# Optimization experiments

Measured on AMD Instinct MI355X. Metric: run time of the kernel, lower is better.

The kernel has to match this reference:

```python
import jax, jax.numpy as jnp
import numpy as np

B, S, D, H = 4, 1024, 2048, 16
HD = D // H
SCALE = float(np.sqrt(HD))


def setup_inputs() -> dict:
    key = jax.random.key(0)
    ks = jax.random.split(key, 11)
    std = 1.0 / np.sqrt(D)
    inp = {
        'q': jax.random.normal(ks[0], (B, S, D), jnp.float32),
        'k': jax.random.normal(ks[1], (B, S, D), jnp.float32),
        'v': jax.random.normal(ks[2], (B, S, D), jnp.float32),
        'wq_w': jax.random.uniform(ks[3], (D, D), jnp.float32, -std, std),
        'wq_b': jax.random.uniform(ks[4], (D,), jnp.float32, -std, std),
        'wk_w': jax.random.uniform(ks[5], (D, D), jnp.float32, -std, std),
        'wk_b': jax.random.uniform(ks[6], (D,), jnp.float32, -std, std),
        'wv_w': jax.random.uniform(ks[7], (D, D), jnp.float32, -std, std),
        'wv_b': jax.random.uniform(ks[8], (D,), jnp.float32, -std, std),
        'wo_w': jax.random.uniform(ks[9], (D, D), jnp.float32, -std, std),
        'wo_b': jax.random.uniform(ks[10], (D,), jnp.float32, -std, std),
    }
    return inp


def reference(q, k, v, wq_w, wq_b, wk_w, wk_b, wv_w, wv_b, wo_w, wo_b):
    # Linear projections (torch Linear: x @ W.T + b), split into heads: [B,H,S,HD]
    Q = (q @ wq_w.T + wq_b).reshape(B, S, H, HD).transpose(0, 2, 1, 3)
    K = (k @ wk_w.T + wk_b).reshape(B, S, H, HD).transpose(0, 2, 1, 3)
    V = (v @ wv_w.T + wv_b).reshape(B, S, H, HD).transpose(0, 2, 1, 3)
    # scaled dot-product attention; mask=None, dropout identity (eval)
    scores = jnp.einsum('bhqd,bhkd->bhqk', Q, K) / SCALE  # [B,H,S,S]
    attn = jax.nn.softmax(scores, axis=-1)
    context = jnp.einsum('bhqk,bhkd->bhqd', attn, V)      # [B,H,S,HD]
    context = context.transpose(0, 2, 1, 3).reshape(B, S, D)
    output = context @ wo_w.T + wo_b
    return output, attn
```

## Files before the change

kernel.cpp:

```cpp
#include <hip/hip_runtime.h>
#include <hip/hip_bf16.h>


typedef __attribute__((ext_vector_type(4)))  float f32x4;
typedef __attribute__((ext_vector_type(16))) float f32x16;
typedef __attribute__((ext_vector_type(8))) short  bf16x8;
typedef __attribute__((ext_vector_type(4))) short  short4v;
typedef __attribute__((ext_vector_type(8))) short  short8v;

__device__ __forceinline__ short f2b(float f) {
  __hip_bfloat16 h = __float2bfloat16(f);
  return __builtin_bit_cast(short, h);
}
__device__ __forceinline__ float b2f(short s) {
  __hip_bfloat16 h = __builtin_bit_cast(__hip_bfloat16, s);
  return __bfloat162float(h);
}

__global__ void cast_all(
    const float* __restrict__ q,  const float* __restrict__ k,  const float* __restrict__ v,
    const float* __restrict__ w0, const float* __restrict__ w1, const float* __restrict__ w2,
    const float* __restrict__ w3,
    __hip_bfloat16* __restrict__ qd, __hip_bfloat16* __restrict__ kd, __hip_bfloat16* __restrict__ vd,
    __hip_bfloat16* __restrict__ d0, __hip_bfloat16* __restrict__ d1, __hip_bfloat16* __restrict__ d2,
    __hip_bfloat16* __restrict__ d3)
{
  const int c0 = blockIdx.x * blockDim.x + threadIdx.x;
#pragma unroll
  for (int it = 0; it < 10; ++it) {
    int c = c0 + it * 524288;
    const float* in; __hip_bfloat16* out; size_t off;
    if (c < 3145728) {
      int seg = c >> 20; off = (size_t)(c & 1048575) * 8;
      in  = seg == 0 ? q  : (seg == 1 ? k  : v);
      out = seg == 0 ? qd : (seg == 1 ? kd : vd);
    } else {
      int c2 = c - 3145728;
      int seg = c2 >> 19; off = (size_t)(c2 & 524287) * 8;
      in  = seg == 0 ? w0 : (seg == 1 ? w1 : (seg == 2 ? w2 : w3));
      out = seg == 0 ? d0 : (seg == 1 ? d1 : (seg == 2 ? d2 : d3));
    }
    float4 a = *(const float4*)(in + off);
    float4 b = *(const float4*)(in + off + 4);
    short8v o;
    o[0] = f2b(a.x); o[1] = f2b(a.y); o[2] = f2b(a.z); o[3] = f2b(a.w);
    o[4] = f2b(b.x); o[5] = f2b(b.y); o[6] = f2b(b.z); o[7] = f2b(b.w);
    *(short8v*)(out + off) = o;
  }
}

__device__ __forceinline__ void gload_lds16(const __hip_bfloat16* g, char* l) {
  __builtin_amdgcn_global_load_lds(
      (const __attribute__((address_space(1))) unsigned int*)g,
      (__attribute__((address_space(3))) unsigned int*)l, 16, 0, 0);
}

template<bool SWAP>
__device__ __forceinline__ void gemm_core64(
    const __hip_bfloat16* ga0, const __hip_bfloat16* gb0,
    char* As, char* Bs, char* lA0, char* lB0,
    int wm, int wn, int l16, int g, f32x4 (&acc)[4][4])
{
  const int sw = (l16 & 7) << 4;
#pragma unroll 1
  for (int kt = 0; kt < 32; ++kt) {
    __syncthreads();
#pragma unroll
    for (int c = 0; c < 4; ++c) {
      gload_lds16(ga0 + c * 16384, lA0 + c * 1024);
      gload_lds16(gb0 + c * 16384, lB0 + c * 1024);
    }
    ga0 += 64; gb0 += 64;
    asm volatile("s_waitcnt vmcnt(0)" ::: "memory");
    __syncthreads();
#pragma unroll
    for (int ks = 0; ks < 2; ++ks) {
      bf16x8 a[4];
#pragma unroll
      for (int mf = 0; mf < 4; ++mf)
        a[mf] = *(const bf16x8*)(As + (wm + mf * 16 + l16) * 128 + ((ks * 64 + g * 16) ^ sw));
#pragma unroll
      for (int nf = 0; nf < 4; ++nf) {
        bf16x8 b = *(const bf16x8*)(Bs + (wn + nf * 16 + l16) * 128 + ((ks * 64 + g * 16) ^ sw));
#pragma unroll
        for (int mf = 0; mf < 4; ++mf) {
          if (SWAP)
            acc[mf][nf] = __builtin_amdgcn_mfma_f32_16x16x32_bf16(b, a[mf], acc[mf][nf], 0, 0, 0);
          else
            acc[mf][nf] = __builtin_amdgcn_mfma_f32_16x16x32_bf16(a[mf], b, acc[mf][nf], 0, 0, 0);
        }
      }
    }
  }
}

__device__ __forceinline__ const __hip_bfloat16* stage_src(
    const __hip_bfloat16* M, int base, int wid, int lane) {
  return M + (size_t)(base + wid * 32 + (lane >> 3)) * 2048
           + (((lane & 7) ^ ((lane >> 3) & 7)) * 8);
}

__global__ __launch_bounds__(256, 3) void gemm_qkv(
    const __hip_bfloat16* __restrict__ qbf, const __hip_bfloat16* __restrict__ kbf,
    const __hip_bfloat16* __restrict__ vbf,
    const __hip_bfloat16* __restrict__ wqb, const __hip_bfloat16* __restrict__ wkb,
    const __hip_bfloat16* __restrict__ wvb,
    const float* __restrict__ bq, const float* __restrict__ bk, const float* __restrict__ bv,
    __hip_bfloat16* __restrict__ Qh, __hip_bfloat16* __restrict__ Kh,
    __hip_bfloat16* __restrict__ Vt)
{
  __shared__ __align__(16) char smem[32768];
  char* As = smem;
  char* Bs = smem + 16384;

  const int z = blockIdx.z;
  const __hip_bfloat16* A  = z == 0 ? qbf : (z == 1 ? kbf : vbf);
  const __hip_bfloat16* Bt = z == 0 ? wqb : (z == 1 ? wkb : wvb);
  const float* bias        = z == 0 ? bq  : (z == 1 ? bk  : bv);
  __hip_bfloat16* C        = z == 0 ? Qh  : (z == 1 ? Kh  : Vt);

  const int tid  = threadIdx.x;
  const int lane = tid & 63, wid = tid >> 6;
  const int l16  = lane & 15, g = lane >> 4;
  const int m0 = blockIdx.y * 128, n0 = blockIdx.x * 128;
  const int wm = (wid >> 1) * 64, wn = (wid & 1) * 64;

  f32x4 acc[4][4];
#pragma unroll
  for (int i = 0; i < 4; ++i)
#pragma unroll
    for (int j = 0; j < 4; ++j) acc[i][j] = f32x4{0.f, 0.f, 0.f, 0.f};

  const __hip_bfloat16* ga0 = stage_src(A,  m0, wid, lane);
  const __hip_bfloat16* gb0 = stage_src(Bt, n0, wid, lane);
  char* lA0 = As + wid * 4096;
  char* lB0 = Bs + wid * 4096;

  if (z == 2) gemm_core64<false>(ga0, gb0, As, Bs, lA0, lB0, wm, wn, l16, g, acc);
  else        gemm_core64<true >(ga0, gb0, As, Bs, lA0, lB0, wm, wn, l16, g, acc);

  const int hh = n0 >> 7, bb = m0 >> 10, sbase = m0 & 1023;
  const int c8 = (tid & 15) * 8;
  char* Cs = smem;
  if (z != 2) {
#pragma unroll
    for (int h = 0; h < 2; ++h) {
      __syncthreads();
      if ((wid >> 1) == h) {
#pragma unroll
        for (int nf = 0; nf < 4; ++nf) {
          f32x4 bvv = *(const f32x4*)(bias + n0 + wn + nf * 16 + g * 4);
#pragma unroll
          for (int mf = 0; mf < 4; ++mf) {
            int sl = mf * 16 + l16;
            int hd = wn + nf * 16 + g * 4;
            short4v pk;
#pragma unroll
            for (int r = 0; r < 4; ++r) pk[r] = f2b(acc[mf][nf][r] + bvv[r]);
            *(short4v*)(Cs + sl * 272 + hd * 2) = pk;
          }
        }
      }
      __syncthreads();
#pragma unroll
      for (int p = 0; p < 4; ++p) {
        int rl = p * 16 + (tid >> 4);
        bf16x8 val = *(const bf16x8*)(Cs + rl * 272 + c8 * 2);
        *(bf16x8*)(C + (((size_t)bb * 16 + hh) * 1024 + sbase + h * 64 + rl) * 128 + c8) = val;
      }
    }
  } else {
#pragma unroll
    for (int h = 0; h < 2; ++h) {
      __syncthreads();
      if ((wid & 1) == h) {
#pragma unroll
        for (int nf = 0; nf < 4; ++nf) {
          float bvv = bias[n0 + wn + nf * 16 + l16];
#pragma unroll
          for (int mf = 0; mf < 4; ++mf) {
            int hdl = nf * 16 + l16;
            int s0  = wm + mf * 16 + g * 4;
            short4v pk;
#pragma unroll
            for (int r = 0; r < 4; ++r) pk[r] = f2b(acc[mf][nf][r] + bvv);
            *(short4v*)(Cs + hdl * 272 + s0 * 2) = pk;
          }
        }
      }
      __syncthreads();
#pragma unroll
      for (int p = 0; p < 4; ++p) {
        int rl = p * 16 + (tid >> 4);
        bf16x8 val = *(const bf16x8*)(Cs + rl * 272 + c8 * 2);
        *(bf16x8*)(C + (((size_t)bb * 16 + hh) * 128 + h * 64 + rl) * 1024 + sbase + c8) = val;
      }
    }
  }
}

__global__ __launch_bounds__(256, 3) void gemm_out(
    const __hip_bfloat16* __restrict__ A, const __hip_bfloat16* __restrict__ Bt,
    const float* __restrict__ bias, float* __restrict__ C)
{
  __shared__ __align__(16) char smem[32768];
  char* As = smem;
  char* Bs = smem + 16384;
  const int tid  = threadIdx.x;
  const int lane = tid & 63, wid = tid >> 6;
  const int l16  = lane & 15, g = lane >> 4;
  const int m0 = blockIdx.y * 128, n0 = blockIdx.x * 128;
  const int wm = (wid >> 1) * 64, wn = (wid & 1) * 64;

  f32x4 acc[4][4];
#pragma unroll
  for (int i = 0; i < 4; ++i)
#pragma unroll
    for (int j = 0; j < 4; ++j) acc[i][j] = f32x4{0.f, 0.f, 0.f, 0.f};

  const __hip_bfloat16* ga0 = stage_src(A,  m0, wid, lane);
  const __hip_bfloat16* gb0 = stage_src(Bt, n0, wid, lane);
  char* lA0 = As + wid * 4096;
  char* lB0 = Bs + wid * 4096;

  gemm_core64<true>(ga0, gb0, As, Bs, lA0, lB0, wm, wn, l16, g, acc);

#pragma unroll
  for (int nf = 0; nf < 4; ++nf) {
    f32x4 bv = *(const f32x4*)(bias + n0 + wn + nf * 16 + g * 4);
#pragma unroll
    for (int mf = 0; mf < 4; ++mf) {
      int m = m0 + wm + mf * 16 + l16;
      int n = n0 + wn + nf * 16 + g * 4;
      f32x4 o;
#pragma unroll
      for (int r = 0; r < 4; ++r) o[r] = acc[mf][nf][r] + bv[r];
      *(f32x4*)(C + (size_t)m * 2048 + n) = o;
    }
  }
}

__global__ __launch_bounds__(512, 4) void attn_kernel(
    const __hip_bfloat16* __restrict__ Qh,
    const __hip_bfloat16* __restrict__ Kh,
    const __hip_bfloat16* __restrict__ Vt,
    float* __restrict__ attn,
    __hip_bfloat16* __restrict__ ctx)
{
  __shared__ __align__(16) char Plds[32 * 2048];
  __shared__ float red[8 * 32];
  __shared__ float invs[32];

  const int tid = threadIdx.x, lane = tid & 63, w = tid >> 6;
  const int l16 = lane & 15, g = lane >> 4;
  const int l31 = lane & 31, kh = lane >> 5;

  const int bid = blockIdx.x;
  const int xcd = bid & 7, j = bid >> 3;
  const int bh  = xcd * 8 + (j >> 5);
  const int q0  = (j & 31) << 5;

  const __hip_bfloat16* Qp = Qh + ((size_t)bh * 1024 + q0) * 128;
  const __hip_bfloat16* Kp = Kh + (size_t)bh * 1024 * 128;
  const __hip_bfloat16* Vp = Vt + (size_t)bh * 128 * 1024;
  float* ap = attn + ((size_t)bh * 1024 + q0) * 1024;

  bf16x8 qb[8];
#pragma unroll
  for (int s = 0; s < 8; ++s)
    qb[s] = *(const bf16x8*)(Qp + (size_t)l31 * 128 + s * 16 + kh * 8);

  const float esc2 = 0.12751744f;
  float rs = 0.f;

#pragma unroll
  for (int pass = 0; pass < 4; ++pass) {
    const int keybase = pass * 256 + w * 32;
    const __hip_bfloat16* kr = Kp + (size_t)(keybase + l31) * 128 + kh * 8;
    bf16x8 kb[8];
#pragma unroll
    for (int s = 0; s < 8; ++s) kb[s] = *(const bf16x8*)(kr + s * 16);
    f32x16 acc;
#pragma unroll
    for (int i = 0; i < 16; ++i) acc[i] = 0.f;
    __builtin_amdgcn_s_setprio(1);
#pragma unroll
    for (int s = 0; s < 8; ++s)
      acc = __builtin_amdgcn_mfma_f32_32x32x16_bf16(kb[s], qb[s], acc, 0, 0, 0);
    __builtin_amdgcn_s_setprio(0);
#pragma unroll
    for (int grp = 0; grp < 4; ++grp) {
      short4v pk;
#pragma unroll
      for (int jj = 0; jj < 4; ++jj) {
        float e = exp2f(acc[grp * 4 + jj] * esc2);
        rs += e;
        pk[jj] = f2b(e);
      }
      int key0 = keybase + grp * 8 + kh * 4;
      *(short4v*)(Plds + l31 * 2048 + ((key0 * 2) ^ ((l31 & 7) << 4))) = pk;
    }
  }
  rs += __shfl_xor(rs, 32, 64);
  if (lane < 32) red[w * 32 + l31] = rs;
  __syncthreads();
  if (tid < 32) {
    float t = 0.f;
#pragma unroll
    for (int ww = 0; ww < 8; ++ww) t += red[ww * 32 + tid];
    invs[tid] = 1.0f / t;
  }

  f32x4 acc2[2];
  acc2[0] = f32x4{0.f, 0.f, 0.f, 0.f};
  acc2[1] = f32x4{0.f, 0.f, 0.f, 0.f};
  {
    const char* pr0 = Plds + l16 * 2048;
    const char* pr1 = Plds + (16 + l16) * 2048;
    const int sw = (l16 & 7) << 4;
#pragma unroll 4
    for (int kt = 0; kt < 32; ++kt) {
      int cb = (kt * 64 + g * 16) ^ sw;
      bf16x8 pa0 = *(const bf16x8*)(pr0 + cb);
      bf16x8 pa1 = *(const bf16x8*)(pr1 + cb);
      const __hip_bfloat16* vr = Vp + (size_t)(16 * w + l16) * 1024 + kt * 32 + g * 8;
      bf16x8 vb = *(const bf16x8*)vr;
      __builtin_amdgcn_s_setprio(1);
      acc2[0] = __builtin_amdgcn_mfma_f32_16x16x32_bf16(pa0, vb, acc2[0], 0, 0, 0);
      acc2[1] = __builtin_amdgcn_mfma_f32_16x16x32_bf16(pa1, vb, acc2[1], 0, 0, 0);
      __builtin_amdgcn_s_setprio(0);
    }
  }
  __syncthreads();

  {
    const int row = 4 * w + g;
    const float invr = invs[row];
    const char* rp = Plds + row * 2048;
    const int sw = (row & 7) << 4;
    float* apr = ap + (size_t)row * 1024;
#pragma unroll
    for (int it = 0; it < 16; ++it) {
      int col = it * 64 + l16 * 4;
      short4v pb = *(const short4v*)(rp + ((col * 2) ^ sw));
      f32x4 val;
#pragma unroll
      for (int r = 0; r < 4; ++r) val[r] = b2f(pb[r]) * invr;
      __builtin_nontemporal_store(val, (f32x4*)(apr + col));
    }
  }
  __syncthreads();

  {
    __hip_bfloat16* cs = (__hip_bfloat16*)Plds;
#pragma unroll
    for (int t = 0; t < 2; ++t) {
      f32x4 iv = *(const f32x4*)(invs + t * 16 + g * 4);
#pragma unroll
      for (int r = 0; r < 4; ++r)
        cs[(t * 16 + g * 4 + r) * 128 + 16 * w + l16] = __float2bfloat16(acc2[t][r] * iv[r]);
    }
    __syncthreads();
    const int row = tid >> 4, c8 = (tid & 15) * 8;
    bf16x8 val = *(const bf16x8*)(cs + row * 128 + c8);
    const int bb = bh >> 4, h = bh & 15;
    *(bf16x8*)(ctx + ((size_t)(bb * 1024 + q0 + row)) * 2048 + h * 128 + c8) = val;
  }
}

extern "C" void kernel_launch(void* const* d_in, const int* in_sizes, int n_in,
                              void* d_out, int out_size, void* d_ws, size_t ws_size,
                              hipStream_t stream) {
  const float* q    = (const float*)d_in[0];
  const float* k    = (const float*)d_in[1];
  const float* v    = (const float*)d_in[2];
  const float* wq_w = (const float*)d_in[3];
  const float* wq_b = (const float*)d_in[4];
  const float* wk_w = (const float*)d_in[5];
  const float* wk_b = (const float*)d_in[6];
  const float* wv_w = (const float*)d_in[7];
  const float* wv_b = (const float*)d_in[8];
  const float* wo_w = (const float*)d_in[9];
  const float* wo_b = (const float*)d_in[10];

  const size_t BSD = (size_t)4 * 1024 * 2048;
  const size_t DD  = (size_t)2048 * 2048;

  float* out  = (float*)d_out;
  float* attn = out + BSD;

  __hip_bfloat16* qbf = (__hip_bfloat16*)attn;
  __hip_bfloat16* kbf = qbf + BSD;
  __hip_bfloat16* vbf = kbf + BSD;

  __hip_bfloat16* wqb = (__hip_bfloat16*)d_ws;
  __hip_bfloat16* wkb = wqb + DD;
  __hip_bfloat16* wvb = wkb + DD;
  __hip_bfloat16* wob = wvb + DD;
  __hip_bfloat16* Qh  = wob + DD;
  __hip_bfloat16* Kh  = Qh + BSD;
  __hip_bfloat16* Vt  = Kh + BSD;
  __hip_bfloat16* ctx = Vt + BSD;

  cast_all<<<2048, 256, 0, stream>>>(q, k, v, wq_w, wk_w, wv_w, wo_w,
                                     qbf, kbf, vbf, wqb, wkb, wvb, wob);

  gemm_qkv<<<dim3(16, 32, 3), dim3(256), 0, stream>>>(
      qbf, kbf, vbf, wqb, wkb, wvb, wq_b, wk_b, wv_b, Qh, Kh, Vt);

  attn_kernel<<<dim3(2048), dim3(512), 0, stream>>>(Qh, Kh, Vt, attn, ctx);

  gemm_out<<<dim3(16, 32), dim3(256), 0, stream>>>(ctx, wob, wo_b, out);
}
```

Measured before the change: 344.0 us.

## Warp-specialize attention tail: half waves do PV MFMA, half stream attn output

Splits the eight waves after softmax so four waves compute the P·V product, each covering 32 output columns with twice the MFMAs, while the other four waves write the normalized attention probabilities to global memory. A separate LDS buffer for the context tile lets both phases run at the same time with one fewer barrier. The aim is to overlap the large attn store with matrix work instead of running them back to back. The cost is about 8KB more LDS per block, which may lower occupancy, and more accumulator registers in the MFMA waves.

```diff
diff --git a/kernel.cpp b/kernel.cpp
--- a/kernel.cpp
+++ b/kernel.cpp
@@ -248,6 +248,7 @@
     __hip_bfloat16* __restrict__ ctx)
 {
   __shared__ __align__(16) char Plds[32 * 2048];
+  __shared__ __align__(16) __hip_bfloat16 cs[32 * 128];
   __shared__ float red[8 * 32];
   __shared__ float invs[32];
 
@@ -310,57 +311,65 @@
     for (int ww = 0; ww < 8; ++ww) t += red[ww * 32 + tid];
     invs[tid] = 1.0f / t;
   }
-
-  f32x4 acc2[2];
-  acc2[0] = f32x4{0.f, 0.f, 0.f, 0.f};
-  acc2[1] = f32x4{0.f, 0.f, 0.f, 0.f};
-  {
+  __syncthreads();
+
+  if (w < 4) {
+    f32x4 acc2[2][2];
+#pragma unroll
+    for (int t = 0; t < 2; ++t)
+#pragma unroll
+      for (int f2 = 0; f2 < 2; ++f2) acc2[t][f2] = f32x4{0.f, 0.f, 0.f, 0.f};
     const char* pr0 = Plds + l16 * 2048;
     const char* pr1 = Plds + (16 + l16) * 2048;
     const int sw = (l16 & 7) << 4;
+    const __hip_bfloat16* vr0 = Vp + (size_t)(32 * w + l16) * 1024;
+    const __hip_bfloat16* vr1 = Vp + (size_t)(32 * w + 16 + l16) * 1024;
 #pragma unroll 4
     for (int kt = 0; kt < 32; ++kt) {
       int cb = (kt * 64 + g * 16) ^ sw;
       bf16x8 pa0 = *(const bf16x8*)(pr0 + cb);
       bf16x8 pa1 = *(const bf16x8*)(pr1 + cb);
-      const __hip_bfloat16* vr = Vp + (size_t)(16 * w + l16) * 1024 + kt * 32 + g * 8;
-      bf16x8 vb = *(const bf16x8*)vr;
+      bf16x8 vb0 = *(const bf16x8*)(vr0 + kt * 32 + g * 8);
+      bf16x8 vb1 = *(const bf16x8*)(vr1 + kt * 32 + g * 8);
       __builtin_amdgcn_s_setprio(1);
-      acc2[0] = __builtin_amdgcn_mfma_f32_16x16x32_bf16(pa0, vb, acc2[0], 0, 0, 0);
-      acc2[1] = __builtin_amdgcn_mfma_f32_16x16x32_bf16(pa1, vb, acc2[1], 0, 0, 0);
+      acc2[0][0] = __builtin_amdgcn_mfma_f32_16x16x32_bf16(pa0, vb0, acc2[0][0], 0, 0, 0);
+      acc2[1][0] = __builtin_amdgcn_mfma_f32_16x16x32_bf16(pa1, vb0, acc2[1][0], 0, 0, 0);
+      acc2[0][1] = __builtin_amdgcn_mfma_f32_16x16x32_bf16(pa0, vb1, acc2[0][1], 0, 0, 0);
+      acc2[1][1] = __builtin_amdgcn_mfma_f32_16x16x32_bf16(pa1, vb1, acc2[1][1], 0, 0, 0);
       __builtin_amdgcn_s_setprio(0);
     }
-  }
-  __syncthreads();
-
-  {
-    const int row = 4 * w + g;
-    const float invr = invs[row];
-    const char* rp = Plds + row * 2048;
-    const int sw = (row & 7) << 4;
-    float* apr = ap + (size_t)row * 1024;
-#pragma unroll
-    for (int it = 0; it < 16; ++it) {
-      int col = it * 64 + l16 * 4;
-      short4v pb = *(const short4v*)(rp + ((col * 2) ^ sw));
-      f32x4 val;
-#pragma unroll
-      for (int r = 0; r < 4; ++r) val[r] = b2f(pb[r]) * invr;
-      __builtin_nontemporal_store(val, (f32x4*)(apr + col));
-    }
-  }
-  __syncthreads();
-
-  {
-    __hip_bfloat16* cs = (__hip_bfloat16*)Plds;
 #pragma unroll
     for (int t = 0; t < 2; ++t) {
       f32x4 iv = *(const f32x4*)(invs + t * 16 + g * 4);
 #pragma unroll
-      for (int r = 0; r < 4; ++r)
-        cs[(t * 16 + g * 4 + r) * 128 + 16 * w + l16] = __float2bfloat16(acc2[t][r] * iv[r]);
-    }
-    __syncthreads();
+      for (int f2 = 0; f2 < 2; ++f2)
+#pragma unroll
+        for (int r = 0; r < 4; ++r)
+          cs[(t * 16 + g * 4 + r) * 128 + 32 * w + f2 * 16 + l16] =
+              __float2bfloat16(acc2[t][f2][r] * iv[r]);
+    }
+  } else {
+#pragma unroll
+    for (int rr = 0; rr < 2; ++rr) {
+      const int row = (w - 4) * 8 + rr * 4 + g;
+      const float invr = invs[row];
+      const char* rp = Plds + row * 2048;
+      const int swr = (row & 7) << 4;
+      float* apr = ap + (size_t)row * 1024;
+#pragma unroll
+      for (int it = 0; it < 16; ++it) {
+        int col = it * 64 + l16 * 4;
+        short4v pb = *(const short4v*)(rp + ((col * 2) ^ swr));
+        f32x4 val;
+#pragma unroll
+        for (int r = 0; r < 4; ++r) val[r] = b2f(pb[r]) * invr;
+        __builtin_nontemporal_store(val, (f32x4*)(apr + col));
+      }
+    }
+  }
+  __syncthreads();
+
+  {
     const int row = tid >> 4, c8 = (tid & 15) * 8;
     bf16x8 val = *(const bf16x8*)(cs + row * 128 + c8);
     const int bb = bh >> 4, h = bh & 15;
```

Measured after the change: 332.9 us. 3.2% less time.
